# Performance work log

Measured on AMD Instinct MI355X. Metric: run time of the kernel, lower is better.

## Reference

```python
import jax, jax.numpy as jnp
import numpy as np

EMBED = 1024
HEADS = 16
INTERNAL = 1024  # embedding_dim // downsample_rate
HEAD_DIM = INTERNAL // HEADS


def setup_inputs() -> dict:
    key = jax.random.key(0)
    ks = jax.random.split(key, 12)
    B, S = 2, 2048
    s_in = 1.0 / np.sqrt(EMBED)
    s_out = 1.0 / np.sqrt(INTERNAL)
    return {
        "queries": jax.random.normal(ks[0], (B, S, EMBED), jnp.float32),
        "keys": jax.random.normal(ks[1], (B, S, EMBED), jnp.float32),
        "values": jax.random.normal(ks[2], (B, S, EMBED), jnp.float32),
        "Wq": jax.random.uniform(ks[3], (EMBED, INTERNAL), jnp.float32, -s_in, s_in),
        "bq": jax.random.uniform(ks[4], (INTERNAL,), jnp.float32, -s_in, s_in),
        "Wk": jax.random.uniform(ks[5], (EMBED, INTERNAL), jnp.float32, -s_in, s_in),
        "bk": jax.random.uniform(ks[6], (INTERNAL,), jnp.float32, -s_in, s_in),
        "Wv": jax.random.uniform(ks[7], (EMBED, INTERNAL), jnp.float32, -s_in, s_in),
        "bv": jax.random.uniform(ks[8], (INTERNAL,), jnp.float32, -s_in, s_in),
        "Wo": jax.random.uniform(ks[9], (INTERNAL, EMBED), jnp.float32, -s_out, s_out),
        "bo": jax.random.uniform(ks[10], (EMBED,), jnp.float32, -s_out, s_out),
    }


def _split_heads(x):
    B, S, D = x.shape
    return x.reshape(B, S, HEADS, D // HEADS).transpose(0, 2, 1, 3)  # bhsd


def reference(queries, keys, values, Wq, bq, Wk, bk, Wv, bv, Wo, bo):
    q = _split_heads(queries @ Wq + bq)
    k = _split_heads(keys @ Wk + bk)
    v = _split_heads(values @ Wv + bv)
    # NOTE: original scales by 1/sqrt(internal_dim), not 1/sqrt(head_dim)
    scale = 1.0 / np.sqrt(INTERNAL).astype(np.float32)
    scores = jnp.einsum("bhqd,bhkd->bhqk", q, k) * scale
    probs = jax.nn.softmax(scores, axis=-1)
    out = jnp.einsum("bhqk,bhkd->bhqd", probs, v)
    B, H, S, Dh = out.shape
    out = out.transpose(0, 2, 1, 3).reshape(B, S, H * Dh)
    return out @ Wo + bo
```

## Files before the change

### kernel.cpp

```cpp
#include <hip/hip_runtime.h>
#include <stdint.h>

typedef unsigned short u16;
typedef __attribute__((ext_vector_type(8))) short short8;
typedef __attribute__((ext_vector_type(4))) float f32x4;
typedef __attribute__((ext_vector_type(16))) float f32x16;
typedef __attribute__((ext_vector_type(8))) unsigned short u16x8;
typedef __attribute__((ext_vector_type(4))) unsigned short u16x4;
typedef __attribute__((ext_vector_type(4))) uint32_t u32x4;

#if __has_builtin(__builtin_amdgcn_exp2f)
#define EXP2(x) __builtin_amdgcn_exp2f(x)
#else
#define EXP2(x) exp2f(x)
#endif

__device__ __forceinline__ u16 f2bf(float f) {
  union { float f; uint32_t u; } v; v.f = f;
  uint32_t r = (v.u + 0x7FFFu + ((v.u >> 16) & 1u)) >> 16;
  return (u16)r;
}

__device__ __forceinline__ float bf2f(u16 u) {
  union { uint32_t u; float f; } v; v.u = ((uint32_t)u) << 16;
  return v.f;
}

__device__ __forceinline__ uint32_t pack2(float a, float b) {
  return (__float_as_uint(b) & 0xffff0000u) | (__float_as_uint(a) >> 16);
}

__device__ __forceinline__ void gload_lds16(const void* g, void* l) {
  __builtin_amdgcn_global_load_lds(
      (const __attribute__((address_space(1))) void*)g,
      (__attribute__((address_space(3))) void*)l,
      16, 0, 0);
}

__device__ __forceinline__ int xcd_swz() {
  int flat = blockIdx.x + gridDim.x * (blockIdx.y + gridDim.y * blockIdx.z);
  int nwg = gridDim.x * gridDim.y * gridDim.z;
  return (flat & 7) * (nwg >> 3) + (flat >> 3);
}

__global__ __launch_bounds__(256) void cvt_x(const float* __restrict__ q,
                                             const float* __restrict__ k,
                                             const float* __restrict__ v,
                                             u16* __restrict__ dst) {
  const float* src = blockIdx.z == 0 ? q : (blockIdx.z == 1 ? k : v);
  u16* d = dst + (size_t)blockIdx.z * (4096u * 1024u);
  size_t i = ((size_t)blockIdx.x * 256 + threadIdx.x) * 8;
  float4 a = *(const float4*)(src + i);
  float4 b = *(const float4*)(src + i + 4);
  u16x8 o;
  o[0] = f2bf(a.x); o[1] = f2bf(a.y); o[2] = f2bf(a.z); o[3] = f2bf(a.w);
  o[4] = f2bf(b.x); o[5] = f2bf(b.y); o[6] = f2bf(b.z); o[7] = f2bf(b.w);
  *(u16x8*)(d + i) = o;
}

__global__ __launch_bounds__(256) void cvt_wt(const float* __restrict__ Wq,
                                              const float* __restrict__ Wk,
                                              const float* __restrict__ Wv,
                                              const float* __restrict__ Wo,
                                              u16* __restrict__ Wt4) {
  const float* W = blockIdx.z == 0 ? Wq : (blockIdx.z == 1 ? Wk
                   : (blockIdx.z == 2 ? Wv : Wo));
  u16* Wt = Wt4 + (size_t)blockIdx.z * (1024u * 1024u);
  __shared__ u16 tile[64][65];
  int kt = blockIdx.x * 64, nt = blockIdx.y * 64;
  int t = threadIdx.x;
#pragma unroll
  for (int r = 0; r < 4; ++r) {
    int id = t + r * 256;
    int kk = id >> 4, c4 = id & 15;
    float4 vv = *(const float4*)(W + (size_t)(kt + kk) * 1024 + nt + c4 * 4);
    tile[kk][c4 * 4 + 0] = f2bf(vv.x);
    tile[kk][c4 * 4 + 1] = f2bf(vv.y);
    tile[kk][c4 * 4 + 2] = f2bf(vv.z);
    tile[kk][c4 * 4 + 3] = f2bf(vv.w);
  }
  __syncthreads();
#pragma unroll
  for (int r = 0; r < 4; ++r) {
    int id = t + r * 256;
    int n = id >> 4, kc = id & 15;
    u16x4 o;
    o[0] = tile[kc * 4 + 0][n];
    o[1] = tile[kc * 4 + 1][n];
    o[2] = tile[kc * 4 + 2][n];
    o[3] = tile[kc * 4 + 3][n];
    *(u16x4*)(Wt + (size_t)(nt + n) * 1024 + kt + kc * 4) = o;
  }
}

template <bool F32OUT>
__device__ __forceinline__ void gemm_tile(const u16* __restrict__ A,
                                          const u16* __restrict__ Bt,
                                          const float* __restrict__ bias,
                                          u16* __restrict__ Cb,
                                          float* __restrict__ Cf,
                                          float scale, int bm, int bn) {
  __shared__ u16 Alds[128 * 64];
  __shared__ u16 Blds[128 * 64];
  const int tid = threadIdx.x;
  const int lane = tid & 63, w = tid >> 6;
  const int wm = (w >> 1) * 64, wn = (w & 1) * 64;
  const int l15 = lane & 15, lg = lane >> 4;

  f32x4 acc[4][4] = {};

  int srow[4], scol[4], soff[4];
#pragma unroll
  for (int i = 0; i < 4; ++i) {
    int o = (w * 4 + i) * 1024 + lane * 16;
    int row = o >> 7;
    int kc = ((o >> 4) & 7) ^ (row & 7);
    srow[i] = row; scol[i] = kc * 8; soff[i] = o;
  }

  for (int kt = 0; kt < 16; ++kt) {
    __syncthreads();
#pragma unroll
    for (int i = 0; i < 4; ++i) {
      gload_lds16(A + (size_t)(bm * 128 + srow[i]) * 1024 + kt * 64 + scol[i],
                  (char*)Alds + soff[i]);
      gload_lds16(Bt + (size_t)(bn * 128 + srow[i]) * 1024 + kt * 64 + scol[i],
                  (char*)Blds + soff[i]);
    }
    __syncthreads();
#pragma unroll
    for (int ks = 0; ks < 2; ++ks) {
      short8 af[4], bf[4];
#pragma unroll
      for (int m = 0; m < 4; ++m) {
        int r = wm + m * 16 + l15;
        int byt = r * 128 + ((ks * 64 + lg * 16) ^ ((r & 7) << 4));
        af[m] = *(const short8*)((const char*)Alds + byt);
      }
#pragma unroll
      for (int n = 0; n < 4; ++n) {
        int r = wn + n * 16 + l15;
        int byt = r * 128 + ((ks * 64 + lg * 16) ^ ((r & 7) << 4));
        bf[n] = *(const short8*)((const char*)Blds + byt);
      }
#pragma unroll
      for (int m = 0; m < 4; ++m)
#pragma unroll
        for (int n = 0; n < 4; ++n)
          acc[m][n] = __builtin_amdgcn_mfma_f32_16x16x32_bf16(
              af[m], bf[n], acc[m][n], 0, 0, 0);
    }
  }
#pragma unroll
  for (int m = 0; m < 4; ++m) {
    int row0 = bm * 128 + wm + m * 16 + lg * 4;
#pragma unroll
    for (int n = 0; n < 4; ++n) {
      int col = bn * 128 + wn + n * 16 + l15;
      float bvv = bias[col];
#pragma unroll
      for (int r = 0; r < 4; ++r) {
        float v = (acc[m][n][r] + bvv) * scale;
        if (F32OUT)
          Cf[(size_t)(row0 + r) * 1024 + col] = v;
        else
          Cb[(size_t)(row0 + r) * 1024 + col] = f2bf(v);
      }
    }
  }
}

__global__ __launch_bounds__(256) void proj_kernel(const u16* __restrict__ X3,
                                                   const u16* __restrict__ Wt3,
                                                   const float* __restrict__ bq,
                                                   const float* __restrict__ bk,
                                                   const float* __restrict__ bv,
                                                   u16* __restrict__ out3) {
  int l = xcd_swz();
  int bm = l & 31, bn = (l >> 5) & 7, z = l >> 8;
  const float* bias = z == 0 ? bq : (z == 1 ? bk : bv);
  float scale = z == 0 ? 0.045084220f : 1.0f;
  gemm_tile<false>(X3 + (size_t)z * 4096 * 1024, Wt3 + (size_t)z * 1024 * 1024,
                   bias, out3 + (size_t)z * 4096 * 1024, nullptr, scale,
                   bm, bn);
}

__global__ __launch_bounds__(256) void outproj_kernel(const u16* __restrict__ Att,
                                                      const u16* __restrict__ Wot,
                                                      const float* __restrict__ bo,
                                                      float* __restrict__ out) {
  int l = xcd_swz();
  int bm = l & 31, bn = l >> 5;
  gemm_tile<true>(Att, Wot, bo, nullptr, out, 1.0f, bm, bn);
}

__global__ __launch_bounds__(256) void vt_kernel(const u16* __restrict__ v,
                                                 u16* __restrict__ vt) {
  int bh = blockIdx.y;
  int sbase = blockIdx.x * 64;
  int b = bh >> 4, h = bh & 15;
  __shared__ u16 tile[64][65];
  int t = threadIdx.x;
#pragma unroll
  for (int r = 0; r < 2; ++r) {
    int id = t + r * 256;
    int s = id >> 3, dc = id & 7;
    u16x8 x = *(const u16x8*)(v + (size_t)(b * 2048 + sbase + s) * 1024 +
                              h * 64 + dc * 8);
#pragma unroll
    for (int j = 0; j < 8; ++j) tile[s][dc * 8 + j] = x[j];
  }
  __syncthreads();
#pragma unroll
  for (int r = 0; r < 2; ++r) {
    int id = t + r * 256;
    int d = id >> 3, sc = id & 7;
    u16x8 o;
#pragma unroll
    for (int j = 0; j < 8; ++j) o[j] = tile[sc * 8 + j][d];
    *(u16x8*)(vt + ((size_t)bh * 64 + d) * 2048 + sbase + sc * 8) = o;
  }
}

__global__ __launch_bounds__(256, 2) void attn_kernel(const u16* __restrict__ q,
                                                      const u16* __restrict__ k,
                                                      const u16* __restrict__ vt,
                                                      u16* __restrict__ attp0,
                                                      u16* __restrict__ attp3,
                                                      float* __restrict__ lp) {
  __shared__ u16 smem[16384];
  const int tid = threadIdx.x, lane = tid & 63, w = tid >> 6;
  const int l31 = lane & 31, hi = lane >> 5;
  int l = xcd_swz();
  const int bx = l & 7, bh = (l >> 3) & 31, z = l >> 8;
  const int b = bh >> 4, h = bh & 15;
  const int qb = bx * 256 + w * 64;

  short8 qf[2][4];
#pragma unroll
  for (int g = 0; g < 2; ++g) {
    const u16* qrow =
        q + (size_t)(b * 2048 + qb + g * 32 + l31) * 1024 + h * 64 + hi * 8;
#pragma unroll
    for (int s = 0; s < 4; ++s) qf[g][s] = *(const short8*)(qrow + s * 16);
  }

  f32x16 acc[2][2] = {};
  float lsum[2] = {0.f, 0.f};

  int scol[2], rowK[2], rowV[2];
#pragma unroll
  for (int i = 0; i < 2; ++i) {
    int gi = i * 256 + tid;
    int row = gi & 63, c16 = gi >> 6;
    scol[i] = c16 * 8;
    rowV[i] = row;
    rowK[i] = row ^ ((((row >> 2) ^ (row >> 3)) & 1) ? 12 : 0);
  }
  const u16* ksrc = k + (size_t)b * 2048 * 1024 + h * 64;
  const u16* vsrc = vt + (size_t)bh * 64 * 2048;
  const int kb0 = z * 512;
  const char* KL = (const char*)smem;
  const char* VL = (const char*)smem + 8192;

  for (int tt = 0; tt < 8; ++tt) {
    const int kbase = kb0 + tt * 64;
    __syncthreads();
#pragma unroll
    for (int i = 0; i < 2; ++i) {
      gload_lds16(ksrc + (size_t)(kbase + rowK[i]) * 1024 + scol[i],
                  (char*)smem + i * 4096 + tid * 16);
      gload_lds16(vsrc + (size_t)rowV[i] * 2048 + kbase + scol[i],
                  (char*)smem + 8192 + i * 4096 + tid * 16);
    }
    __syncthreads();

#pragma unroll
    for (int kg = 0; kg < 2; ++kg) {
      short8 ak[4], bv[4];
#pragma unroll
      for (int s = 0; s < 4; ++s)
        ak[s] = *(const short8*)(KL + (s * 2 + hi) * 1024 +
                                 (kg * 32 + l31) * 16);
#pragma unroll
      for (int c = 0; c < 2; ++c)
#pragma unroll
        for (int half = 0; half < 2; ++half)
          bv[c * 2 + half] =
              *(const short8*)(VL + (kg * 4 + c * 2 + hi) * 1024 +
                               (half * 32 + l31) * 16);
#pragma unroll
      for (int g = 0; g < 2; ++g) {
        f32x16 sc = {};
#pragma unroll
        for (int s = 0; s < 4; ++s)
          sc = __builtin_amdgcn_mfma_f32_32x32x16_bf16(ak[s], qf[g][s], sc,
                                                       0, 0, 0);
        float p[16];
#pragma unroll
        for (int e = 0; e < 16; ++e) p[e] = EXP2(sc[e]);
#pragma unroll
        for (int e = 0; e < 16; e += 4)
          lsum[g] += (p[e] + p[e + 1]) + (p[e + 2] + p[e + 3]);
#pragma unroll
        for (int c = 0; c < 2; ++c) {
          u32x4 fw;
          fw[0] = pack2(p[8 * c + 0], p[8 * c + 1]);
          fw[1] = pack2(p[8 * c + 2], p[8 * c + 3]);
          fw[2] = pack2(p[8 * c + 4], p[8 * c + 5]);
          fw[3] = pack2(p[8 * c + 6], p[8 * c + 7]);
          short8 pf = __builtin_bit_cast(short8, fw);
          acc[g][0] = __builtin_amdgcn_mfma_f32_32x32x16_bf16(
              pf, bv[c * 2 + 0], acc[g][0], 0, 0, 0);
          acc[g][1] = __builtin_amdgcn_mfma_f32_32x32x16_bf16(
              pf, bv[c * 2 + 1], acc[g][1], 0, 0, 0);
        }
      }
    }
  }

  float lt[2];
#pragma unroll
  for (int g = 0; g < 2; ++g) lt[g] = lsum[g] + __shfl_xor(lsum[g], 32);
  if (hi == 0) {
    float* lbase = lp + (size_t)z * 65536;
#pragma unroll
    for (int g = 0; g < 2; ++g)
      lbase[(size_t)(b * 2048 + qb + g * 32 + l31) * 16 + h] = lt[g];
  }

  __syncthreads();
  u16* tw = smem + w * 4096;
#pragma unroll
  for (int g = 0; g < 2; ++g)
#pragma unroll
    for (int r = 0; r < 16; ++r) {
      int rq = (r & 3) + 8 * (r >> 2) + 4 * hi;
      int row = g * 32 + rq;
      tw[row * 64 + l31] = f2bf(acc[g][0][r]);
      tw[row * 64 + 32 + l31] = f2bf(acc[g][1][r]);
    }
  asm volatile("s_waitcnt lgkmcnt(0)" ::: "memory");
  __builtin_amdgcn_sched_barrier(0);
  u16* pbase = (z == 3) ? attp3 : (attp0 + (size_t)z * (4096u * 1024u));
  u16* abase = pbase + (size_t)(b * 2048 + qb) * 1024 + h * 64;
#pragma unroll
  for (int i = 0; i < 8; ++i) {
    int id = lane + i * 64;
    int row = id >> 3, ch = id & 7;
    u16x8 vv = *(const u16x8*)(tw + row * 64 + ch * 8);
    *(u16x8*)(abase + (size_t)row * 1024 + ch * 8) = vv;
  }
}

__global__ __launch_bounds__(256) void merge_kernel(const u16* __restrict__ p012,
                                                    const u16* __restrict__ p3,
                                                    const float* __restrict__ lp,
                                                    u16* __restrict__ out) {
  const size_t SZX = (size_t)4096 * 1024;
  size_t i0 = ((size_t)blockIdx.x * 256 + threadIdx.x) * 8;
  int row = (int)(i0 >> 10);
  int head = (int)((i0 >> 6) & 15);
  size_t li = (size_t)row * 16 + head;
  float lsm = (lp[li] + lp[65536 + li]) + (lp[2 * 65536 + li] + lp[3 * 65536 + li]);
  float rinv = 1.0f / lsm;
  u16x8 x0 = *(const u16x8*)(p012 + i0);
  u16x8 x1 = *(const u16x8*)(p012 + SZX + i0);
  u16x8 x2 = *(const u16x8*)(p012 + 2 * SZX + i0);
  u16x8 x3 = *(const u16x8*)(p3 + i0);
  u16x8 o;
#pragma unroll
  for (int j = 0; j < 8; ++j)
    o[j] = f2bf(((bf2f(x0[j]) + bf2f(x1[j])) + (bf2f(x2[j]) + bf2f(x3[j]))) *
                rinv);
  *(u16x8*)(out + i0) = o;
}

extern "C" void kernel_launch(void* const* d_in, const int* in_sizes, int n_in,
                              void* d_out, int out_size, void* d_ws,
                              size_t ws_size, hipStream_t stream) {
  const float* Q  = (const float*)d_in[0];
  const float* K  = (const float*)d_in[1];
  const float* V  = (const float*)d_in[2];
  const float* Wq = (const float*)d_in[3];
  const float* bq = (const float*)d_in[4];
  const float* Wk = (const float*)d_in[5];
  const float* bk = (const float*)d_in[6];
  const float* Wv = (const float*)d_in[7];
  const float* bv = (const float*)d_in[8];
  const float* Wo = (const float*)d_in[9];
  const float* bo = (const float*)d_in[10];
  float* out = (float*)d_out;

  u16* ws = (u16*)d_ws;
  const size_t SZX = (size_t)4096 * 1024;
  const size_t SZW = (size_t)1024 * 1024;
  u16* Xbf   = ws;
  u16* Wtbf  = ws + 3 * SZX;
  u16* QKVbf = Wtbf + 4 * SZW;
  u16* VTbf  = QKVbf + 3 * SZX;
  u16* ATTbf = VTbf + SZX;
  u16*   attP012 = Xbf;
  u16*   attP3   = (u16*)d_out;
  float* lsumP   = out + 2 * 1024 * 1024;

  hipLaunchKernelGGL(cvt_x, dim3(2048, 1, 3), dim3(256), 0, stream, Q, K, V,
                     Xbf);
  hipLaunchKernelGGL(cvt_wt, dim3(16, 16, 4), dim3(256), 0, stream, Wq, Wk, Wv,
                     Wo, Wtbf);
  hipLaunchKernelGGL(proj_kernel, dim3(32, 8, 3), dim3(256), 0, stream, Xbf,
                     Wtbf, bq, bk, bv, QKVbf);
  hipLaunchKernelGGL(vt_kernel, dim3(32, 32), dim3(256), 0, stream,
                     QKVbf + 2 * SZX, VTbf);
  hipLaunchKernelGGL(attn_kernel, dim3(8, 32, 4), dim3(256), 0, stream, QKVbf,
                     QKVbf + SZX, VTbf, attP012, attP3, lsumP);
  hipLaunchKernelGGL(merge_kernel, dim3(2048), dim3(256), 0, stream, attP012,
                     attP3, lsumP, ATTbf);
  hipLaunchKernelGGL(outproj_kernel, dim3(32, 8), dim3(256), 0, stream, ATTbf,
                     Wtbf + 3 * SZW, bo, out);
}
```

Measured before the change: 133.5 us.

## Triple-buffer K/V loads in attention and halve the key-split count

The attention kernel now prefetches K/V tiles two steps ahead into a three-slot LDS ring, so global loads overlap MFMA compute instead of waiting at each tile. The key split drops from 4 to 2 partitions, each covering 1024 keys, so the grid halves and the merge kernel reads two partials instead of four. The trade-off is half as many blocks, which may lower occupancy and parallelism, and 48KB of LDS per block, which may limit blocks per CU. An explicit vmcnt wait was also added before the barrier in the projection GEMM.

```diff
diff --git a/kernel.cpp b/kernel.cpp
--- a/kernel.cpp
+++ b/kernel.cpp
@@ -127,6 +127,7 @@
       gload_lds16(Bt + (size_t)(bn * 128 + srow[i]) * 1024 + kt * 64 + scol[i],
                   (char*)Blds + soff[i]);
     }
+    asm volatile("s_waitcnt vmcnt(0)" ::: "memory");
     __syncthreads();
 #pragma unroll
     for (int ks = 0; ks < 2; ++ks) {
@@ -225,10 +226,9 @@
 __global__ __launch_bounds__(256, 2) void attn_kernel(const u16* __restrict__ q,
                                                       const u16* __restrict__ k,
                                                       const u16* __restrict__ vt,
-                                                      u16* __restrict__ attp0,
-                                                      u16* __restrict__ attp3,
+                                                      u16* __restrict__ attp,
                                                       float* __restrict__ lp) {
-  __shared__ u16 smem[16384];
+  __shared__ u16 smem[24576];
   const int tid = threadIdx.x, lane = tid & 63, w = tid >> 6;
   const int l31 = lane & 31, hi = lane >> 5;
   int l = xcd_swz();
@@ -259,21 +259,33 @@
   }
   const u16* ksrc = k + (size_t)b * 2048 * 1024 + h * 64;
   const u16* vsrc = vt + (size_t)bh * 64 * 2048;
-  const int kb0 = z * 512;
-  const char* KL = (const char*)smem;
-  const char* VL = (const char*)smem + 8192;
-
-  for (int tt = 0; tt < 8; ++tt) {
-    const int kbase = kb0 + tt * 64;
-    __syncthreads();
+  const int kb0 = z * 1024;
+
+  auto stage = [&](int tile, int buf) {
+    const int kbase = kb0 + tile * 64;
+    char* dst = (char*)smem + buf * 16384;
 #pragma unroll
     for (int i = 0; i < 2; ++i) {
       gload_lds16(ksrc + (size_t)(kbase + rowK[i]) * 1024 + scol[i],
-                  (char*)smem + i * 4096 + tid * 16);
+                  dst + i * 4096 + tid * 16);
       gload_lds16(vsrc + (size_t)rowV[i] * 2048 + kbase + scol[i],
-                  (char*)smem + 8192 + i * 4096 + tid * 16);
-    }
+                  dst + 8192 + i * 4096 + tid * 16);
+    }
+  };
+
+  stage(0, 0);
+  stage(1, 1);
+
+  for (int tt = 0; tt < 16; ++tt) {
+    if (tt < 15)
+      asm volatile("s_waitcnt vmcnt(4)" ::: "memory");
+    else
+      asm volatile("s_waitcnt vmcnt(0)" ::: "memory");
     __syncthreads();
+    if (tt + 2 < 16) stage(tt + 2, (tt + 2) % 3);
+
+    const char* KL = (const char*)smem + (tt % 3) * 16384;
+    const char* VL = KL + 8192;
 
 #pragma unroll
     for (int kg = 0; kg < 2; ++kg) {
@@ -342,8 +354,8 @@
     }
   asm volatile("s_waitcnt lgkmcnt(0)" ::: "memory");
   __builtin_amdgcn_sched_barrier(0);
-  u16* pbase = (z == 3) ? attp3 : (attp0 + (size_t)z * (4096u * 1024u));
-  u16* abase = pbase + (size_t)(b * 2048 + qb) * 1024 + h * 64;
+  u16* abase = attp + (size_t)z * (4096u * 1024u) +
+               (size_t)(b * 2048 + qb) * 1024 + h * 64;
 #pragma unroll
   for (int i = 0; i < 8; ++i) {
     int id = lane + i * 64;
@@ -353,8 +365,7 @@
   }
 }
 
-__global__ __launch_bounds__(256) void merge_kernel(const u16* __restrict__ p012,
-                                                    const u16* __restrict__ p3,
+__global__ __launch_bounds__(256) void merge_kernel(const u16* __restrict__ p01,
                                                     const float* __restrict__ lp,
                                                     u16* __restrict__ out) {
   const size_t SZX = (size_t)4096 * 1024;
@@ -362,17 +373,14 @@
   int row = (int)(i0 >> 10);
   int head = (int)((i0 >> 6) & 15);
   size_t li = (size_t)row * 16 + head;
-  float lsm = (lp[li] + lp[65536 + li]) + (lp[2 * 65536 + li] + lp[3 * 65536 + li]);
+  float lsm = lp[li] + lp[65536 + li];
   float rinv = 1.0f / lsm;
-  u16x8 x0 = *(const u16x8*)(p012 + i0);
-  u16x8 x1 = *(const u16x8*)(p012 + SZX + i0);
-  u16x8 x2 = *(const u16x8*)(p012 + 2 * SZX + i0);
-  u16x8 x3 = *(const u16x8*)(p3 + i0);
+  u16x8 x0 = *(const u16x8*)(p01 + i0);
+  u16x8 x1 = *(const u16x8*)(p01 + SZX + i0);
   u16x8 o;
 #pragma unroll
   for (int j = 0; j < 8; ++j)
-    o[j] = f2bf(((bf2f(x0[j]) + bf2f(x1[j])) + (bf2f(x2[j]) + bf2f(x3[j]))) *
-                rinv);
+    o[j] = f2bf((bf2f(x0[j]) + bf2f(x1[j])) * rinv);
   *(u16x8*)(out + i0) = o;
 }
 
@@ -400,9 +408,8 @@
   u16* QKVbf = Wtbf + 4 * SZW;
   u16* VTbf  = QKVbf + 3 * SZX;
   u16* ATTbf = VTbf + SZX;
-  u16*   attP012 = Xbf;
-  u16*   attP3   = (u16*)d_out;
-  float* lsumP   = out + 2 * 1024 * 1024;
+  u16*   attP  = Xbf;
+  float* lsumP = (float*)(Xbf + 2 * SZX);
 
   hipLaunchKernelGGL(cvt_x, dim3(2048, 1, 3), dim3(256), 0, stream, Q, K, V,
                      Xbf);
@@ -412,10 +419,10 @@
                      Wtbf, bq, bk, bv, QKVbf);
   hipLaunchKernelGGL(vt_kernel, dim3(32, 32), dim3(256), 0, stream,
                      QKVbf + 2 * SZX, VTbf);
-  hipLaunchKernelGGL(attn_kernel, dim3(8, 32, 4), dim3(256), 0, stream, QKVbf,
-                     QKVbf + SZX, VTbf, attP012, attP3, lsumP);
-  hipLaunchKernelGGL(merge_kernel, dim3(2048), dim3(256), 0, stream, attP012,
-                     attP3, lsumP, ATTbf);
+  hipLaunchKernelGGL(attn_kernel, dim3(8, 32, 2), dim3(256), 0, stream, QKVbf,
+                     QKVbf + SZX, VTbf, attP, lsumP);
+  hipLaunchKernelGGL(merge_kernel, dim3(2048), dim3(256), 0, stream, attP,
+                     lsumP, ATTbf);
   hipLaunchKernelGGL(outproj_kernel, dim3(32, 8), dim3(256), 0, stream, ATTbf,
                      Wtbf + 3 * SZW, bo, out);
 }
```

After: 125.2 us. 1.07x faster.

## Multi-buffer LDS staging in GEMM and attention kernels to overlap loads with MFMA

Applied to the files above, without the earlier changes.

The projection GEMM tile now double-buffers its A/B LDS tiles and issues the next k-tile's global-to-LDS loads before computing the current one. The attention kernel gains a triple-buffered K/V LDS ring with two tiles in flight, using explicit vmcnt waits. The aim is to hide global load latency behind MFMA work. The GEMM kernels also drop the XCD-swizzled block mapping in favour of plain blockIdx, which may change L2 locality. The extra LDS footprint (64KB for GEMM, 48KB for attention) could lower occupancy.

```diff
diff --git a/kernel.cpp b/kernel.cpp
--- a/kernel.cpp
+++ b/kernel.cpp
@@ -100,8 +100,8 @@
                                           u16* __restrict__ Cb,
                                           float* __restrict__ Cf,
                                           float scale, int bm, int bn) {
-  __shared__ u16 Alds[128 * 64];
-  __shared__ u16 Blds[128 * 64];
+  __shared__ u16 Alds[2][128 * 64];
+  __shared__ u16 Blds[2][128 * 64];
   const int tid = threadIdx.x;
   const int lane = tid & 63, w = tid >> 6;
   const int wm = (w >> 1) * 64, wn = (w & 1) * 64;
@@ -118,16 +118,24 @@
     srow[i] = row; scol[i] = kc * 8; soff[i] = o;
   }
 
-  for (int kt = 0; kt < 16; ++kt) {
-    __syncthreads();
+  auto stage = [&](int kt, int buf) {
 #pragma unroll
     for (int i = 0; i < 4; ++i) {
       gload_lds16(A + (size_t)(bm * 128 + srow[i]) * 1024 + kt * 64 + scol[i],
-                  (char*)Alds + soff[i]);
+                  (char*)Alds[buf] + soff[i]);
       gload_lds16(Bt + (size_t)(bn * 128 + srow[i]) * 1024 + kt * 64 + scol[i],
-                  (char*)Blds + soff[i]);
-    }
+                  (char*)Blds[buf] + soff[i]);
+    }
+  };
+
+  stage(0, 0);
+
+  for (int kt = 0; kt < 16; ++kt) {
+    asm volatile("s_waitcnt vmcnt(0)" ::: "memory");
     __syncthreads();
+    if (kt + 1 < 16) stage(kt + 1, (kt + 1) & 1);
+    const char* AL = (const char*)Alds[kt & 1];
+    const char* BL = (const char*)Blds[kt & 1];
 #pragma unroll
     for (int ks = 0; ks < 2; ++ks) {
       short8 af[4], bf[4];
@@ -135,13 +143,13 @@
       for (int m = 0; m < 4; ++m) {
         int r = wm + m * 16 + l15;
         int byt = r * 128 + ((ks * 64 + lg * 16) ^ ((r & 7) << 4));
-        af[m] = *(const short8*)((const char*)Alds + byt);
+        af[m] = *(const short8*)(AL + byt);
       }
 #pragma unroll
       for (int n = 0; n < 4; ++n) {
         int r = wn + n * 16 + l15;
         int byt = r * 128 + ((ks * 64 + lg * 16) ^ ((r & 7) << 4));
-        bf[n] = *(const short8*)((const char*)Blds + byt);
+        bf[n] = *(const short8*)(BL + byt);
       }
 #pragma unroll
       for (int m = 0; m < 4; ++m)
@@ -176,8 +184,7 @@
                                                    const float* __restrict__ bk,
                                                    const float* __restrict__ bv,
                                                    u16* __restrict__ out3) {
-  int l = xcd_swz();
-  int bm = l & 31, bn = (l >> 5) & 7, z = l >> 8;
+  int bm = blockIdx.x, bn = blockIdx.y, z = blockIdx.z;
   const float* bias = z == 0 ? bq : (z == 1 ? bk : bv);
   float scale = z == 0 ? 0.045084220f : 1.0f;
   gemm_tile<false>(X3 + (size_t)z * 4096 * 1024, Wt3 + (size_t)z * 1024 * 1024,
@@ -189,8 +196,7 @@
                                                       const u16* __restrict__ Wot,
                                                       const float* __restrict__ bo,
                                                       float* __restrict__ out) {
-  int l = xcd_swz();
-  int bm = l & 31, bn = l >> 5;
+  int bm = blockIdx.x, bn = blockIdx.y;
   gemm_tile<true>(Att, Wot, bo, nullptr, out, 1.0f, bm, bn);
 }
 
@@ -228,7 +234,7 @@
                                                       u16* __restrict__ attp0,
                                                       u16* __restrict__ attp3,
                                                       float* __restrict__ lp) {
-  __shared__ u16 smem[16384];
+  __shared__ u16 smem[24576];
   const int tid = threadIdx.x, lane = tid & 63, w = tid >> 6;
   const int l31 = lane & 31, hi = lane >> 5;
   int l = xcd_swz();
@@ -260,20 +266,32 @@
   const u16* ksrc = k + (size_t)b * 2048 * 1024 + h * 64;
   const u16* vsrc = vt + (size_t)bh * 64 * 2048;
   const int kb0 = z * 512;
-  const char* KL = (const char*)smem;
-  const char* VL = (const char*)smem + 8192;
-
-  for (int tt = 0; tt < 8; ++tt) {
-    const int kbase = kb0 + tt * 64;
-    __syncthreads();
+
+  auto stage = [&](int tile, int buf) {
+    const int kbase = kb0 + tile * 64;
+    char* dst = (char*)smem + buf * 16384;
 #pragma unroll
     for (int i = 0; i < 2; ++i) {
       gload_lds16(ksrc + (size_t)(kbase + rowK[i]) * 1024 + scol[i],
-                  (char*)smem + i * 4096 + tid * 16);
+                  dst + i * 4096 + tid * 16);
       gload_lds16(vsrc + (size_t)rowV[i] * 2048 + kbase + scol[i],
-                  (char*)smem + 8192 + i * 4096 + tid * 16);
-    }
+                  dst + 8192 + i * 4096 + tid * 16);
+    }
+  };
+
+  stage(0, 0);
+  stage(1, 1);
+
+  for (int tt = 0; tt < 8; ++tt) {
+    if (tt < 7)
+      asm volatile("s_waitcnt vmcnt(4)" ::: "memory");
+    else
+      asm volatile("s_waitcnt vmcnt(0)" ::: "memory");
     __syncthreads();
+    if (tt + 2 < 8) stage(tt + 2, (tt + 2) % 3);
+
+    const char* KL = (const char*)smem + (tt % 3) * 16384;
+    const char* VL = KL + 8192;
 
 #pragma unroll
     for (int kg = 0; kg < 2; ++kg) {
```

New measurement: 136.5 us. 2.2% more time.
